# Performance work log

Measured on AMD Instinct MI355X. Metric: run time of the kernel, lower is better.

Reference implementation:

```python
import jax, jax.numpy as jnp
import numpy as np

B, S, D, H = 2, 2048, 1024, 16
HD = D // H  # head_dim = 64
SCALE = HD ** -0.5


def setup_inputs() -> dict:
    key = jax.random.key(0)
    k1, k2, k3 = jax.random.split(key, 3)
    src = jax.random.normal(k1, (B, S, D), dtype=jnp.float32)
    w_qkv = jax.random.normal(k2, (D, 3 * D), dtype=jnp.float32) * (D ** -0.5)
    b_qkv = jax.random.normal(k3, (3 * D,), dtype=jnp.float32) * 0.02
    return {"src": src, "w_qkv": w_qkv, "b_qkv": b_qkv}


def reference(src, w_qkv, b_qkv):
    # qkv projection: [B,S,3D]
    qkv = src @ w_qkv + b_qkv
    q, k, v = jnp.split(qkv, 3, axis=-1)
    # [B,S,D] -> [B,H,S,HD]
    def heads(x):
        return x.reshape(B, S, H, HD).transpose(0, 2, 1, 3)
    q, k, v = heads(q), heads(k), heads(v)
    # scaled dot-product attention (note: original scales AFTER q@k.T)
    attn = jnp.einsum('bhqd,bhkd->bhqk', q, k) * SCALE
    attn = jax.nn.softmax(attn, axis=-1)
    out = jnp.einsum('bhqk,bhkd->bhqd', attn, v)  # [B,H,S,HD]
    return out.transpose(0, 2, 1, 3).reshape(B, S, D)
```

## Files before the change

kernel.cpp:

```cpp
#include <hip/hip_runtime.h>
#include <hip/hip_bf16.h>

typedef short short8 __attribute__((ext_vector_type(8)));
typedef float f32x4 __attribute__((ext_vector_type(4)));
typedef float f32x16 __attribute__((ext_vector_type(16)));
typedef __hip_bfloat16 bf16;


__device__ __forceinline__ void glds16(const void* g, void* l) {
  __builtin_amdgcn_global_load_lds((const __attribute__((address_space(1))) unsigned int*)g,
                                   (__attribute__((address_space(3))) unsigned int*)l, 16, 0, 0);
}

__device__ __forceinline__ uint pk2(float a, float b) {
  union { bf16 h2[2]; uint u; } pk;
  pk.h2[0] = __float2bfloat16(a);
  pk.h2[1] = __float2bfloat16(b);
  return pk.u;
}

__global__ __launch_bounds__(256) void cvt_src_kernel(const float4* __restrict__ in,
                                                      bf16* __restrict__ out, int n4) {
  int i = blockIdx.x * 256 + threadIdx.x;
  if (i >= n4) return;
  float4 v = in[i];
  union { bf16 h[4]; uint2 u; } pk;
  pk.h[0] = __float2bfloat16(v.x);
  pk.h[1] = __float2bfloat16(v.y);
  pk.h[2] = __float2bfloat16(v.z);
  pk.h[3] = __float2bfloat16(v.w);
  *(uint2*)(out + (size_t)i * 4) = pk.u;
}

__global__ __launch_bounds__(256) void transpose_w_kernel(const float* __restrict__ w,
                                                          bf16* __restrict__ wt) {
  __shared__ float tile[32][33];
  int x0 = blockIdx.x * 32;
  int y0 = blockIdx.y * 32;
  int tx = threadIdx.x & 31, ty = threadIdx.x >> 5;
#pragma unroll
  for (int i = 0; i < 4; i++) {
    int y = ty + i * 8;
    tile[y][tx] = w[(size_t)(y0 + y) * 3072 + x0 + tx];
  }
  __syncthreads();
#pragma unroll
  for (int i = 0; i < 4; i++) {
    int y = ty + i * 8;
    wt[(size_t)(x0 + y) * 1024 + y0 + tx] = __float2bfloat16(tile[tx][y]);
  }
}

__global__ __launch_bounds__(256) void qkv_gemm_kernel(
    const bf16* __restrict__ A, const bf16* __restrict__ Bt,
    const float* __restrict__ bias,
    bf16* __restrict__ q_ws, bf16* __restrict__ k_ws, bf16* __restrict__ vt_ws) {
  __shared__ alignas(16) char AB[32768];
  const int tid = threadIdx.x;
  const int lane = tid & 63, wid = tid >> 6;
  const int lr = lane & 15, lg = lane >> 4;
  const int wm = wid >> 1, wn = wid & 1;
  const int m0 = blockIdx.x * 128, n0 = blockIdx.y * 128;

  const f32x4 z4 = {0.f, 0.f, 0.f, 0.f};
  f32x4 acc[4][4];
#pragma unroll
  for (int m = 0; m < 4; m++)
#pragma unroll
    for (int n = 0; n < 4; n++) acc[m][n] = z4;

  const int srow = lane >> 3;
  const int sseg = (lane & 7) ^ srow;
  const char* Ag = (const char*)A + (size_t)(m0 + wid * 32 + srow) * 2048 + sseg * 16;
  const char* Bg = (const char*)Bt + (size_t)(n0 + wid * 32 + srow) * 2048 + sseg * 16;
  char* Al = AB + wid * 4096;
  char* Bl = AB + 16384 + wid * 4096;
  const int xora = (lr & 7) << 4;

  for (int kt = 0; kt < 16; kt++) {
    __syncthreads();
#pragma unroll
    for (int c = 0; c < 4; c++) {
      glds16(Ag + (size_t)kt * 128 + c * 16384, Al + c * 1024);
      glds16(Bg + (size_t)kt * 128 + c * 16384, Bl + c * 1024);
    }
    asm volatile("s_waitcnt vmcnt(0)" ::: "memory");
    __syncthreads();
#pragma unroll
    for (int g = 0; g < 2; g++) {
      short8 af[4], bfr[4];
#pragma unroll
      for (int m = 0; m < 4; m++)
        af[m] = *(const short8*)(AB + (wm * 64 + m * 16 + lr) * 128 +
                                 ((g * 64 + lg * 16) ^ xora));
#pragma unroll
      for (int n = 0; n < 4; n++)
        bfr[n] = *(const short8*)(AB + 16384 + (wn * 64 + n * 16 + lr) * 128 +
                                  ((g * 64 + lg * 16) ^ xora));
#pragma unroll
      for (int m = 0; m < 4; m++)
#pragma unroll
        for (int n = 0; n < 4; n++)
          acc[m][n] = __builtin_amdgcn_mfma_f32_16x16x32_bf16(af[m], bfr[n], acc[m][n], 0, 0, 0);
    }
  }

  const int which = n0 >> 10;
#pragma unroll
  for (int m = 0; m < 4; m++) {
    int row = m0 + wm * 64 + m * 16 + lg * 4;
    int b = row >> 11;
    int ss0 = row & 2047;
#pragma unroll
    for (int n = 0; n < 4; n++) {
      int col = n0 + wn * 64 + n * 16 + lr;
      int d = col & 1023;
      int h = d >> 6, hd = d & 63;
      size_t bh = (size_t)(b * 16 + h);
      float bv = bias[col];
      if (which == 2) {
        union { bf16 h4[4]; uint2 u; } pk;
#pragma unroll
        for (int r = 0; r < 4; r++) pk.h4[r] = __float2bfloat16(acc[m][n][r] + bv);
        *(uint2*)&vt_ws[(bh * 64 + hd) * 2048 + ss0] = pk.u;
      } else {
        bf16* dst = (which == 0) ? q_ws : k_ws;
#pragma unroll
        for (int r = 0; r < 4; r++)
          dst[(bh * 2048 + (ss0 + r)) * 64 + hd] = __float2bfloat16(acc[m][n][r] + bv);
      }
    }
  }
}

__global__ __launch_bounds__(512) void attn3_kernel(
    const bf16* __restrict__ q_ws, const bf16* __restrict__ k_ws,
    const bf16* __restrict__ vt_ws, float* __restrict__ out) {
  __shared__ alignas(16) char smem[65536];
  const int tid = threadIdx.x;
  const int lane = tid & 63, wid = tid >> 6;
  const int lq = lane & 31, hi = lane >> 5;
  const int hi16 = hi * 16;
  const int xorv = (lq & 7) << 4;
  const float scale_l2e = 0.125f * 1.44269504088896f;

  const int f = blockIdx.x;
  const int bh = (f & 7) * 4 + ((f >> 3) & 3);
  const int qb = f >> 5;
  const int b = bh >> 4, h = bh & 15;
  const int q0 = qb * 256 + wid * 32;

  short8 qf[4];
  {
    const bf16* qrow = q_ws + ((size_t)bh * 2048 + q0 + lq) * 64;
#pragma unroll
    for (int s = 0; s < 4; s++) qf[s] = *(const short8*)(qrow + s * 16 + hi * 8);
  }

  const int l8 = lane >> 3;
  const int segk = (lane & 7) ^ l8;
  const char* kgl = (const char*)k_ws + (size_t)bh * 262144 +
                    (size_t)(wid * 16 + l8) * 128 + segk * 16;
  const int l16 = lane >> 4;
  const int d0v = (wid * 2 + 0) * 4 + l16;
  const int d1v = (wid * 2 + 1) * 4 + l16;
  const char* vg0 = (const char*)vt_ws + (size_t)bh * 262144 + (size_t)d0v * 4096 +
                    (((lane & 15) ^ (d0v & 15)) << 4);
  const char* vg1 = (const char*)vt_ws + (size_t)bh * 262144 + (size_t)d1v * 4096 +
                    (((lane & 15) ^ (d1v & 15)) << 4);

  f32x16 o0a, o0b, o1a, o1b;
#pragma unroll
  for (int r = 0; r < 16; r++) { o0a[r] = 0.f; o0b[r] = 0.f; o1a[r] = 0.f; o1b[r] = 0.f; }
  float m = -1e30f, l = 0.f;

  glds16(kgl, smem + wid * 2048);
  glds16(kgl + 1024, smem + wid * 2048 + 1024);
  glds16(vg0, smem + 32768 + wid * 2048);
  glds16(vg1, smem + 32768 + wid * 2048 + 1024);
  asm volatile("s_waitcnt vmcnt(0)" ::: "memory");
  __builtin_amdgcn_s_barrier();

  for (int kt = 0; kt < 16; ++kt) {
    const int kb_off = (kt & 1) * 16384;
    const int vb_off = 32768 + (kt & 1) * 16384;
    if (kt + 1 < 16) {
      const int nb = ((kt + 1) & 1) * 16384;
      glds16(kgl + (size_t)(kt + 1) * 16384, smem + nb + wid * 2048);
      glds16(kgl + (size_t)(kt + 1) * 16384 + 1024, smem + nb + wid * 2048 + 1024);
      glds16(vg0 + (size_t)(kt + 1) * 256, smem + 32768 + nb + wid * 2048);
      glds16(vg1 + (size_t)(kt + 1) * 256, smem + 32768 + nb + wid * 2048 + 1024);
    }

    f32x16 s0, s1, s2, s3;
#pragma unroll
    for (int r = 0; r < 16; r++) { s0[r] = 0.f; s1[r] = 0.f; s2[r] = 0.f; s3[r] = 0.f; }
#pragma unroll
    for (int st = 0; st < 4; st++) {
      const int doff = (st * 32 + hi16) ^ xorv;
      short8 ka = *(const short8*)(smem + kb_off + lq * 128 + doff);
      short8 kb = *(const short8*)(smem + kb_off + (lq + 32) * 128 + doff);
      short8 kc = *(const short8*)(smem + kb_off + (lq + 64) * 128 + doff);
      short8 kd = *(const short8*)(smem + kb_off + (lq + 96) * 128 + doff);
      __builtin_amdgcn_s_setprio(1);
      s0 = __builtin_amdgcn_mfma_f32_32x32x16_bf16(ka, qf[st], s0, 0, 0, 0);
      s1 = __builtin_amdgcn_mfma_f32_32x32x16_bf16(kb, qf[st], s1, 0, 0, 0);
      s2 = __builtin_amdgcn_mfma_f32_32x32x16_bf16(kc, qf[st], s2, 0, 0, 0);
      s3 = __builtin_amdgcn_mfma_f32_32x32x16_bf16(kd, qf[st], s3, 0, 0, 0);
      __builtin_amdgcn_s_setprio(0);
    }

    float mx[16];
#pragma unroll
    for (int i = 0; i < 16; i++)
      mx[i] = fmaxf(fmaxf(s0[i], s1[i]), fmaxf(s2[i], s3[i]));
#pragma unroll
    for (int i = 0; i < 8; i++) mx[i] = fmaxf(mx[i], mx[i + 8]);
#pragma unroll
    for (int i = 0; i < 4; i++) mx[i] = fmaxf(mx[i], mx[i + 4]);
    float pm = fmaxf(fmaxf(mx[0], mx[1]), fmaxf(mx[2], mx[3]));
    pm = fmaxf(pm, __shfl_xor(pm, 32));
    pm *= scale_l2e;
    if (pm > m + 8.f) {
      float rs = __builtin_amdgcn_exp2f(m - pm);
      m = pm; l *= rs;
#pragma unroll
      for (int r = 0; r < 16; r++) {
        o0a[r] *= rs; o0b[r] *= rs; o1a[r] *= rs; o1b[r] *= rs;
      }
    }
#pragma unroll
    for (int r = 0; r < 16; r++) {
      s0[r] = __builtin_amdgcn_exp2f(__builtin_fmaf(s0[r], scale_l2e, -m));
      s1[r] = __builtin_amdgcn_exp2f(__builtin_fmaf(s1[r], scale_l2e, -m));
      s2[r] = __builtin_amdgcn_exp2f(__builtin_fmaf(s2[r], scale_l2e, -m));
      s3[r] = __builtin_amdgcn_exp2f(__builtin_fmaf(s3[r], scale_l2e, -m));
    }
    {
      float sm[16];
#pragma unroll
      for (int i = 0; i < 16; i++) sm[i] = (s0[i] + s1[i]) + (s2[i] + s3[i]);
#pragma unroll
      for (int i = 0; i < 8; i++) sm[i] += sm[i + 8];
#pragma unroll
      for (int i = 0; i < 4; i++) sm[i] += sm[i + 4];
      float ps = (sm[0] + sm[1]) + (sm[2] + sm[3]);
      ps += __shfl_xor(ps, 32);
      l += ps;
    }

#define PV_KB(S, KB, OA, OB)                                                     \
  {                                                                              \
    uint w0 = pk2(S[0], S[1]), w1 = pk2(S[2], S[3]);                             \
    uint w2 = pk2(S[4], S[5]), w3 = pk2(S[6], S[7]);                             \
    uint w4 = pk2(S[8], S[9]), w5 = pk2(S[10], S[11]);                           \
    uint w6 = pk2(S[12], S[13]), w7 = pk2(S[14], S[15]);                         \
    uint r0 = (uint)__shfl_xor((int)(hi ? w0 : w2), 32);                         \
    uint r1 = (uint)__shfl_xor((int)(hi ? w1 : w3), 32);                         \
    uint r2 = (uint)__shfl_xor((int)(hi ? w4 : w6), 32);                         \
    uint r3 = (uint)__shfl_xor((int)(hi ? w5 : w7), 32);                         \
    union { uint u[4]; short8 s8; } ua, ub;                                      \
    ua.u[0] = hi ? r0 : w0; ua.u[1] = hi ? r1 : w1;                              \
    ua.u[2] = hi ? w2 : r0; ua.u[3] = hi ? w3 : r1;                              \
    ub.u[0] = hi ? r2 : w4; ub.u[1] = hi ? r3 : w5;                              \
    ub.u[2] = hi ? w6 : r2; ub.u[3] = hi ? w7 : r3;                              \
    const int c0 = (((KB) * 4 + hi) ^ (lq & 15)) << 4;                           \
    const int c1 = (((KB) * 4 + 2 + hi) ^ (lq & 15)) << 4;                       \
    short8 va0 = *(const short8*)(smem + vb_off + lq * 256 + c0);                \
    short8 va1 = *(const short8*)(smem + vb_off + (lq + 32) * 256 + c0);         \
    short8 vb0 = *(const short8*)(smem + vb_off + lq * 256 + c1);                \
    short8 vb1 = *(const short8*)(smem + vb_off + (lq + 32) * 256 + c1);         \
    __builtin_amdgcn_s_setprio(1);                                               \
    OA = __builtin_amdgcn_mfma_f32_32x32x16_bf16(va0, ua.s8, OA, 0, 0, 0);       \
    OB = __builtin_amdgcn_mfma_f32_32x32x16_bf16(va1, ua.s8, OB, 0, 0, 0);       \
    OA = __builtin_amdgcn_mfma_f32_32x32x16_bf16(vb0, ub.s8, OA, 0, 0, 0);       \
    OB = __builtin_amdgcn_mfma_f32_32x32x16_bf16(vb1, ub.s8, OB, 0, 0, 0);       \
    __builtin_amdgcn_s_setprio(0);                                               \
  }
    PV_KB(s0, 0, o0a, o1a)
    PV_KB(s1, 1, o0b, o1b)
    PV_KB(s2, 2, o0a, o1a)
    PV_KB(s3, 3, o0b, o1b)
#undef PV_KB

    if (kt < 15) {
      asm volatile("s_waitcnt vmcnt(0)" ::: "memory");
      __builtin_amdgcn_s_barrier();
    }
  }
  __syncthreads();

  f32x16 o0, o1;
#pragma unroll
  for (int r = 0; r < 16; r++) { o0[r] = o0a[r] + o0b[r]; o1[r] = o1a[r] + o1b[r]; }
  float* ep = (float*)(smem) + wid * 1024;
  const float invl = 1.f / l;
  const int eq = lane >> 1, eds = lane & 1;
  float* obase = out + ((size_t)b * 2048 + qb * 256 + wid * 32 + eq) * 1024 +
                 h * 64 + eds * 16;
#pragma unroll
  for (int db = 0; db < 2; db++) {
#pragma unroll
    for (int r = 0; r < 16; r++) {
      int d = (r & 3) + 8 * (r >> 2) + 4 * hi;
      float v = (db ? o1[r] : o0[r]) * invl;
      ep[lq * 32 + ((d + lq) & 31)] = v;
    }
#pragma unroll
    for (int c = 0; c < 4; c++) {
      float4 t;
      t.x = ep[eq * 32 + ((eds * 16 + 4 * c + 0 + eq) & 31)];
      t.y = ep[eq * 32 + ((eds * 16 + 4 * c + 1 + eq) & 31)];
      t.z = ep[eq * 32 + ((eds * 16 + 4 * c + 2 + eq) & 31)];
      t.w = ep[eq * 32 + ((eds * 16 + 4 * c + 3 + eq) & 31)];
      *(float4*)(obase + db * 32 + 4 * c) = t;
    }
  }
}

extern "C" void kernel_launch(void* const* d_in, const int* in_sizes, int n_in,
                              void* d_out, int out_size, void* d_ws, size_t ws_size,
                              hipStream_t stream) {
  (void)in_sizes; (void)n_in; (void)out_size; (void)ws_size;
  const float* src  = (const float*)d_in[0];
  const float* w    = (const float*)d_in[1];
  const float* bias = (const float*)d_in[2];
  float* out = (float*)d_out;

  char* ws = (char*)d_ws;
  bf16* src_bf = (bf16*)ws;
  bf16* wt_bf  = (bf16*)(ws + 8388608);
  bf16* q_ws   = (bf16*)(ws + 8388608 + 6291456);
  bf16* k_ws   = q_ws + 4194304;
  bf16* vt_ws  = k_ws + 4194304;

  cvt_src_kernel<<<4096, 256, 0, stream>>>((const float4*)src, src_bf, 1048576);
  transpose_w_kernel<<<dim3(96, 32), 256, 0, stream>>>(w, wt_bf);
  qkv_gemm_kernel<<<dim3(32, 24), 256, 0, stream>>>(src_bf, wt_bf, bias, q_ws, k_ws, vt_ws);
  attn3_kernel<<<256, 512, 0, stream>>>(q_ws, k_ws, vt_ws, out);
}
```

Before: 102.7 us.

## Merge prep kernels and load K/V directly from global in attention

The src conversion and weight transpose kernels are fused into one launch, saving a kernel launch and letting both run concurrently. The attention kernel drops its double-buffered LDS staging of K and V tiles and the per-iteration barriers, so each wave reads K and V fragments straight from global memory through the cache. This removes LDS traffic and synchronisation, but every wave now fetches K/V independently with no explicit prefetch, which risks exposing global-memory latency and raising L2 traffic.

Measured after the change: 161.0 us. +56.8%, slower.

```diff
diff --git a/kernel.cpp b/kernel.cpp
--- a/kernel.cpp
+++ b/kernel.cpp
@@ -19,35 +19,37 @@
   return pk.u;
 }
 
-__global__ __launch_bounds__(256) void cvt_src_kernel(const float4* __restrict__ in,
-                                                      bf16* __restrict__ out, int n4) {
-  int i = blockIdx.x * 256 + threadIdx.x;
-  if (i >= n4) return;
-  float4 v = in[i];
-  union { bf16 h[4]; uint2 u; } pk;
-  pk.h[0] = __float2bfloat16(v.x);
-  pk.h[1] = __float2bfloat16(v.y);
-  pk.h[2] = __float2bfloat16(v.z);
-  pk.h[3] = __float2bfloat16(v.w);
-  *(uint2*)(out + (size_t)i * 4) = pk.u;
-}
-
-__global__ __launch_bounds__(256) void transpose_w_kernel(const float* __restrict__ w,
-                                                          bf16* __restrict__ wt) {
+__global__ __launch_bounds__(256) void prep_kernel(const float4* __restrict__ in,
+                                                   bf16* __restrict__ src_bf,
+                                                   const float* __restrict__ w,
+                                                   bf16* __restrict__ wt) {
   __shared__ float tile[32][33];
-  int x0 = blockIdx.x * 32;
-  int y0 = blockIdx.y * 32;
-  int tx = threadIdx.x & 31, ty = threadIdx.x >> 5;
-#pragma unroll
-  for (int i = 0; i < 4; i++) {
-    int y = ty + i * 8;
-    tile[y][tx] = w[(size_t)(y0 + y) * 3072 + x0 + tx];
-  }
-  __syncthreads();
-#pragma unroll
-  for (int i = 0; i < 4; i++) {
-    int y = ty + i * 8;
-    wt[(size_t)(x0 + y) * 1024 + y0 + tx] = __float2bfloat16(tile[tx][y]);
+  const int bid = blockIdx.x;
+  if (bid < 4096) {
+    int i = bid * 256 + threadIdx.x;
+    float4 v = in[i];
+    union { bf16 h[4]; uint2 u; } pk;
+    pk.h[0] = __float2bfloat16(v.x);
+    pk.h[1] = __float2bfloat16(v.y);
+    pk.h[2] = __float2bfloat16(v.z);
+    pk.h[3] = __float2bfloat16(v.w);
+    *(uint2*)(src_bf + (size_t)i * 4) = pk.u;
+  } else {
+    int id = bid - 4096;
+    int x0 = (id % 96) * 32;
+    int y0 = (id / 96) * 32;
+    int tx = threadIdx.x & 31, ty = threadIdx.x >> 5;
+#pragma unroll
+    for (int i = 0; i < 4; i++) {
+      int y = ty + i * 8;
+      tile[y][tx] = w[(size_t)(y0 + y) * 3072 + x0 + tx];
+    }
+    __syncthreads();
+#pragma unroll
+    for (int i = 0; i < 4; i++) {
+      int y = ty + i * 8;
+      wt[(size_t)(x0 + y) * 1024 + y0 + tx] = __float2bfloat16(tile[tx][y]);
+    }
   }
 }
 
@@ -133,15 +135,13 @@
   }
 }
 
-__global__ __launch_bounds__(512) void attn3_kernel(
+__global__ __launch_bounds__(512) void attn5_kernel(
     const bf16* __restrict__ q_ws, const bf16* __restrict__ k_ws,
     const bf16* __restrict__ vt_ws, float* __restrict__ out) {
-  __shared__ alignas(16) char smem[65536];
+  __shared__ alignas(16) float eps[8 * 1024];
   const int tid = threadIdx.x;
   const int lane = tid & 63, wid = tid >> 6;
   const int lq = lane & 31, hi = lane >> 5;
-  const int hi16 = hi * 16;
-  const int xorv = (lq & 7) << 4;
   const float scale_l2e = 0.125f * 1.44269504088896f;
 
   const int f = blockIdx.x;
@@ -157,51 +157,28 @@
     for (int s = 0; s < 4; s++) qf[s] = *(const short8*)(qrow + s * 16 + hi * 8);
   }
 
-  const int l8 = lane >> 3;
-  const int segk = (lane & 7) ^ l8;
-  const char* kgl = (const char*)k_ws + (size_t)bh * 262144 +
-                    (size_t)(wid * 16 + l8) * 128 + segk * 16;
-  const int l16 = lane >> 4;
-  const int d0v = (wid * 2 + 0) * 4 + l16;
-  const int d1v = (wid * 2 + 1) * 4 + l16;
-  const char* vg0 = (const char*)vt_ws + (size_t)bh * 262144 + (size_t)d0v * 4096 +
-                    (((lane & 15) ^ (d0v & 15)) << 4);
-  const char* vg1 = (const char*)vt_ws + (size_t)bh * 262144 + (size_t)d1v * 4096 +
-                    (((lane & 15) ^ (d1v & 15)) << 4);
+  const char* kq = (const char*)k_ws + (size_t)bh * 262144 + lq * 128 + hi * 16;
+  const char* vq = (const char*)vt_ws + (size_t)bh * 262144 + (size_t)lq * 4096 + hi * 16;
 
   f32x16 o0a, o0b, o1a, o1b;
 #pragma unroll
   for (int r = 0; r < 16; r++) { o0a[r] = 0.f; o0b[r] = 0.f; o1a[r] = 0.f; o1b[r] = 0.f; }
   float m = -1e30f, l = 0.f;
 
-  glds16(kgl, smem + wid * 2048);
-  glds16(kgl + 1024, smem + wid * 2048 + 1024);
-  glds16(vg0, smem + 32768 + wid * 2048);
-  glds16(vg1, smem + 32768 + wid * 2048 + 1024);
-  asm volatile("s_waitcnt vmcnt(0)" ::: "memory");
-  __builtin_amdgcn_s_barrier();
-
   for (int kt = 0; kt < 16; ++kt) {
-    const int kb_off = (kt & 1) * 16384;
-    const int vb_off = 32768 + (kt & 1) * 16384;
-    if (kt + 1 < 16) {
-      const int nb = ((kt + 1) & 1) * 16384;
-      glds16(kgl + (size_t)(kt + 1) * 16384, smem + nb + wid * 2048);
-      glds16(kgl + (size_t)(kt + 1) * 16384 + 1024, smem + nb + wid * 2048 + 1024);
-      glds16(vg0 + (size_t)(kt + 1) * 256, smem + 32768 + nb + wid * 2048);
-      glds16(vg1 + (size_t)(kt + 1) * 256, smem + 32768 + nb + wid * 2048 + 1024);
-    }
+    const char* kb_ = kq + (size_t)kt * 16384;
+    const char* vb_ = vq + (size_t)kt * 256;
 
     f32x16 s0, s1, s2, s3;
 #pragma unroll
     for (int r = 0; r < 16; r++) { s0[r] = 0.f; s1[r] = 0.f; s2[r] = 0.f; s3[r] = 0.f; }
 #pragma unroll
     for (int st = 0; st < 4; st++) {
-      const int doff = (st * 32 + hi16) ^ xorv;
-      short8 ka = *(const short8*)(smem + kb_off + lq * 128 + doff);
-      short8 kb = *(const short8*)(smem + kb_off + (lq + 32) * 128 + doff);
-      short8 kc = *(const short8*)(smem + kb_off + (lq + 64) * 128 + doff);
-      short8 kd = *(const short8*)(smem + kb_off + (lq + 96) * 128 + doff);
+      const int ko = st * 32;
+      short8 ka = *(const short8*)(kb_ + ko);
+      short8 kb = *(const short8*)(kb_ + 4096 + ko);
+      short8 kc = *(const short8*)(kb_ + 8192 + ko);
+      short8 kd = *(const short8*)(kb_ + 12288 + ko);
       __builtin_amdgcn_s_setprio(1);
       s0 = __builtin_amdgcn_mfma_f32_32x32x16_bf16(ka, qf[st], s0, 0, 0, 0);
       s1 = __builtin_amdgcn_mfma_f32_32x32x16_bf16(kb, qf[st], s1, 0, 0, 0);
@@ -264,12 +241,10 @@
     ua.u[2] = hi ? w2 : r0; ua.u[3] = hi ? w3 : r1;                              \
     ub.u[0] = hi ? r2 : w4; ub.u[1] = hi ? r3 : w5;                              \
     ub.u[2] = hi ? w6 : r2; ub.u[3] = hi ? w7 : r3;                              \
-    const int c0 = (((KB) * 4 + hi) ^ (lq & 15)) << 4;                           \
-    const int c1 = (((KB) * 4 + 2 + hi) ^ (lq & 15)) << 4;                       \
-    short8 va0 = *(const short8*)(smem + vb_off + lq * 256 + c0);                \
-    short8 va1 = *(const short8*)(smem + vb_off + (lq + 32) * 256 + c0);         \
-    short8 vb0 = *(const short8*)(smem + vb_off + lq * 256 + c1);                \
-    short8 vb1 = *(const short8*)(smem + vb_off + (lq + 32) * 256 + c1);         \
+    short8 va0 = *(const short8*)(vb_ + (KB) * 64);                              \
+    short8 va1 = *(const short8*)(vb_ + 131072 + (KB) * 64);                     \
+    short8 vb0 = *(const short8*)(vb_ + (KB) * 64 + 32);                         \
+    short8 vb1 = *(const short8*)(vb_ + 131072 + (KB) * 64 + 32);                \
     __builtin_amdgcn_s_setprio(1);                                               \
     OA = __builtin_amdgcn_mfma_f32_32x32x16_bf16(va0, ua.s8, OA, 0, 0, 0);       \
     OB = __builtin_amdgcn_mfma_f32_32x32x16_bf16(va1, ua.s8, OB, 0, 0, 0);       \
@@ -282,18 +257,12 @@
     PV_KB(s2, 2, o0a, o1a)
     PV_KB(s3, 3, o0b, o1b)
 #undef PV_KB
-
-    if (kt < 15) {
-      asm volatile("s_waitcnt vmcnt(0)" ::: "memory");
-      __builtin_amdgcn_s_barrier();
-    }
-  }
-  __syncthreads();
+  }
 
   f32x16 o0, o1;
 #pragma unroll
   for (int r = 0; r < 16; r++) { o0[r] = o0a[r] + o0b[r]; o1[r] = o1a[r] + o1b[r]; }
-  float* ep = (float*)(smem) + wid * 1024;
+  float* ep = eps + wid * 1024;
   const float invl = 1.f / l;
   const int eq = lane >> 1, eds = lane & 1;
   float* obase = out + ((size_t)b * 2048 + qb * 256 + wid * 32 + eq) * 1024 +
@@ -334,8 +303,7 @@
   bf16* k_ws   = q_ws + 4194304;
   bf16* vt_ws  = k_ws + 4194304;
 
-  cvt_src_kernel<<<4096, 256, 0, stream>>>((const float4*)src, src_bf, 1048576);
-  transpose_w_kernel<<<dim3(96, 32), 256, 0, stream>>>(w, wt_bf);
+  prep_kernel<<<7168, 256, 0, stream>>>((const float4*)src, src_bf, w, wt_bf);
   qkv_gemm_kernel<<<dim3(32, 24), 256, 0, stream>>>(src_bf, wt_bf, bias, q_ws, k_ws, vt_ws);
-  attn3_kernel<<<256, 512, 0, stream>>>(q_ws, k_ws, vt_ws, out);
-}
+  attn5_kernel<<<256, 512, 0, stream>>>(q_ws, k_ws, vt_ws, out);
+}
```
